# Kernel tuning notes

Hardware: AMD Instinct MI355X
Metric: run time of the kernel (lower is better)

The kernel has to match this reference:

```python
import jax, jax.numpy as jnp
import numpy as np

EPS = float(np.finfo(np.float32).eps)
LAMBDA = 0.01          # lambda_coeff
W_POS, W_NEG = 0.7, 0.3  # weights[0], weights[1]
BETA = 1.0             # function_dict['beta'] for 'exp'
N_GROUPS = 64          # number of categorical tuples
GROUP_W = 16           # width of each tuple (tup[1]-tup[0])
CAT_COLS = N_GROUPS * GROUP_W   # 1024 columns covered by tuples
HIDDEN, IN_FEATS = 1024, 2048   # model.layers[0].weight shape
BATCH = 8388608


def setup_inputs() -> dict:
    key = jax.random.key(0)
    k1, k2, k3 = jax.random.split(key, 3)
    p = jax.random.uniform(k1, (BATCH,), jnp.float32)
    y = (jax.random.uniform(k2, (BATCH,), jnp.float32) > 0.5).astype(jnp.float32)
    W = jax.random.normal(k3, (HIDDEN, IN_FEATS), jnp.float32) * 0.05
    return {"p": p, "y": y, "W": W}


def _f(x):
    # 'exp' penalty: 1 - exp(-x^2/beta) + |x|
    return 1.0 - jnp.exp(-(x * x) / BETA) + jnp.abs(x)


def reference(p, y, W):
    # weighted binary cross entropy with clamped probabilities
    log_p = jnp.log(jnp.clip(p, EPS, 1.0 - EPS))
    log_1mp = jnp.log(jnp.clip(1.0 - p, EPS, 1.0 - EPS))
    nll = -(W_POS * y * log_p + W_NEG * (1.0 - y) * log_1mp)
    bce = jnp.mean(nll)

    # per-column L2 norms of first-layer weight: [IN_FEATS]
    col_norm = jnp.sqrt(jnp.sum(W * W, axis=0))

    # tuple groups: mean of column norms within each group, then penalty f
    seg_ids = jnp.repeat(jnp.arange(N_GROUPS), GROUP_W)  # [CAT_COLS]
    group_mean = jax.ops.segment_sum(col_norm[:CAT_COLS], seg_ids,
                                     num_segments=N_GROUPS) / GROUP_W
    reg = jnp.sum(_f(group_mean)) + jnp.sum(_f(col_norm[CAT_COLS:]))

    return bce + reg * LAMBDA
```

## Files before the change

### kernel.cpp

```cpp
#include <hip/hip_runtime.h>
#include <math.h>

#define EPSC 1.1920928955078125e-07f
#define BATCH 8388608
#define IN_FEATS 2048
#define N_W_BLOCKS 128
#define N_BCE_BLOCKS 2048
#define N_SLOTS (N_W_BLOCKS + N_BCE_BLOCKS)
#define TOTAL_BLOCKS (1 + N_SLOTS)
#define BCE_ITERS 4
#define MAGIC 0x5EEDF00Du

__device__ __forceinline__ float penalty_f(float x) {
    return 1.0f - __expf(-x * x) + fabsf(x);
}

__device__ __forceinline__ float wave_reduce(float v) {
    #pragma unroll
    for (int o = 32; o > 0; o >>= 1) v += __shfl_down(v, o, 64);
    return v;
}

__device__ __forceinline__ void publish(unsigned long long* slot, float v) {
    unsigned long long w = ((unsigned long long)MAGIC << 32) | (unsigned long long)__float_as_uint(v);
    __hip_atomic_store(slot, w, __ATOMIC_RELAXED, __HIP_MEMORY_SCOPE_AGENT);
}

__global__ __launch_bounds__(256) void fused_k(
        const float* __restrict__ p, const float* __restrict__ y,
        const float* __restrict__ W,
        unsigned long long* __restrict__ slots,
        float* __restrict__ out) {
    const int b = blockIdx.x;
    const int t = threadIdx.x;

    if (b == 0) {
        float reg = 0.0f, bce = 0.0f;
        #pragma unroll
        for (int j = 0; j < (N_SLOTS + 255) / 256; ++j) {
            int i = t + j * 256;
            if (i < N_SLOTS) {
                unsigned long long w;
                do {
                    w = __hip_atomic_load(&slots[i], __ATOMIC_RELAXED,
                                          __HIP_MEMORY_SCOPE_AGENT);
                } while ((unsigned)(w >> 32) != MAGIC);
                float v = __uint_as_float((unsigned)(w & 0xFFFFFFFFu));
                if (i < N_W_BLOCKS) reg += v; else bce += v;
            }
        }
        reg = wave_reduce(reg);
        bce = wave_reduce(bce);
        __shared__ float wr[4], wb[4];
        if ((t & 63) == 0) { wr[t >> 6] = reg; wb[t >> 6] = bce; }
        __syncthreads();
        if (t == 0) {
            float R = (wr[0] + wr[1]) + (wr[2] + wr[3]);
            float B = (wb[0] + wb[1]) + (wb[2] + wb[3]);
            out[0] = B * (1.0f / (float)BATCH) + 0.01f * R;
        }
    } else if (b <= N_W_BLOCKS) {
        const int sb = b - 1;
        const int colbase = sb * 16;
        const int c4 = t & 3;
        const int rs = t >> 2;
        const float4* wbase = (const float4*)(W + (size_t)rs * IN_FEATS + colbase) + c4;
        float4 a = {0.f, 0.f, 0.f, 0.f};
        #pragma unroll
        for (int it = 0; it < 16; ++it) {
            float4 w = wbase[(size_t)it * 64 * (IN_FEATS / 4)];
            a.x = fmaf(w.x, w.x, a.x);
            a.y = fmaf(w.y, w.y, a.y);
            a.z = fmaf(w.z, w.z, a.z);
            a.w = fmaf(w.w, w.w, a.w);
        }
        __shared__ float lds[64][16];
        lds[rs][c4 * 4 + 0] = a.x;
        lds[rs][c4 * 4 + 1] = a.y;
        lds[rs][c4 * 4 + 2] = a.z;
        lds[rs][c4 * 4 + 3] = a.w;
        __syncthreads();

        __shared__ float ln[16];
        if (t < 16) {
            float s = 0.0f;
            #pragma unroll 8
            for (int r = 0; r < 64; ++r) s += lds[r][t];
            ln[t] = sqrtf(s);
        }
        __syncthreads();
        if (t == 0) {
            float contrib;
            if (sb < 64) {
                float gs = 0.0f;
                #pragma unroll
                for (int k = 0; k < 16; ++k) gs += ln[k];
                contrib = penalty_f(gs * (1.0f / 16.0f));
            } else {
                float s = 0.0f;
                #pragma unroll
                for (int k = 0; k < 16; ++k) s += penalty_f(ln[k]);
                contrib = s;
            }
            publish(&slots[sb], contrib);
        }
    } else {
        const int bb = b - 1 - N_W_BLOCKS;
        const float4* p4 = (const float4*)p + (size_t)bb * 1024;
        const float4* y4 = (const float4*)y + (size_t)bb * 1024;

        float4 pv[BCE_ITERS], yv[BCE_ITERS];
        #pragma unroll
        for (int it = 0; it < BCE_ITERS; ++it) {
            int i = it * 256 + t;
            pv[it] = p4[i];
            yv[it] = y4[i];
        }
        float acc = 0.0f;
        #pragma unroll
        for (int it = 0; it < BCE_ITERS; ++it) {
            float pp[4] = {pv[it].x, pv[it].y, pv[it].z, pv[it].w};
            float yy[4] = {yv[it].x, yv[it].y, yv[it].z, yv[it].w};
            #pragma unroll
            for (int k = 0; k < 4; ++k) {
                bool pos = yy[k] > 0.5f;
                float x  = pos ? pp[k] : 1.0f - pp[k];
                float w  = pos ? 0.7f : 0.3f;
                float xc = fminf(fmaxf(x, EPSC), 1.0f - EPSC);
                acc -= w * __logf(xc);
            }
        }
        acc = wave_reduce(acc);
        __shared__ float ws_[4];
        if ((t & 63) == 0) ws_[t >> 6] = acc;
        __syncthreads();
        if (t == 0) publish(&slots[N_W_BLOCKS + bb], ws_[0] + ws_[1] + ws_[2] + ws_[3]);
    }
}

extern "C" void kernel_launch(void* const* d_in, const int* in_sizes, int n_in,
                              void* d_out, int out_size, void* d_ws, size_t ws_size,
                              hipStream_t stream) {
    const float* p = (const float*)d_in[0];
    const float* y = (const float*)d_in[1];
    const float* W = (const float*)d_in[2];
    float* out = (float*)d_out;
    unsigned long long* slots = (unsigned long long*)d_ws;

    fused_k<<<TOTAL_BLOCKS, 256, 0, stream>>>(p, y, W, slots, out);
}
```

Before: 18.88 us.

## Split weight column-norm work into row-quarter blocks with cross-block partial handoff

The weight-norm stage is reorganised from 128 blocks each covering 16 columns over all rows into 256 blocks, each covering 32 columns over a quarter of the rows. Three of every four blocks publish per-column partial sums of squares to workspace slots, and the fourth polls for them and computes the norms and penalty. The goal is more memory-level parallelism per block, with loads issued up front so W is streamed by more blocks at once. Loads of W, p and y are also made nontemporal. The change adds inter-block spin-waits, which could stall if the finishing blocks are scheduled before their producers.

After: 15.37 us, median of 2. 1.23x faster.

```diff
diff --git a/kernel.cpp b/kernel.cpp
--- a/kernel.cpp
+++ b/kernel.cpp
@@ -1,13 +1,15 @@
 #include <hip/hip_runtime.h>
 #include <math.h>
+
+typedef float f32x4 __attribute__((ext_vector_type(4)));
 
 #define EPSC 1.1920928955078125e-07f
 #define BATCH 8388608
 #define IN_FEATS 2048
-#define N_W_BLOCKS 128
+#define N_STRIPS 64
+#define N_WQ_BLOCKS (N_STRIPS * 4)
 #define N_BCE_BLOCKS 2048
-#define N_SLOTS (N_W_BLOCKS + N_BCE_BLOCKS)
-#define TOTAL_BLOCKS (1 + N_SLOTS)
+#define TOTAL_BLOCKS (1 + N_WQ_BLOCKS + N_BCE_BLOCKS)
 #define BCE_ITERS 4
 #define MAGIC 0x5EEDF00Du
 
@@ -22,14 +24,25 @@
 }
 
 __device__ __forceinline__ void publish(unsigned long long* slot, float v) {
-    unsigned long long w = ((unsigned long long)MAGIC << 32) | (unsigned long long)__float_as_uint(v);
+    unsigned long long w = ((unsigned long long)MAGIC << 32)
+                         | (unsigned long long)__float_as_uint(v);
     __hip_atomic_store(slot, w, __ATOMIC_RELAXED, __HIP_MEMORY_SCOPE_AGENT);
+}
+
+__device__ __forceinline__ float poll(const unsigned long long* slot) {
+    unsigned long long w;
+    do {
+        w = __hip_atomic_load(slot, __ATOMIC_RELAXED, __HIP_MEMORY_SCOPE_AGENT);
+    } while ((unsigned)(w >> 32) != MAGIC);
+    return __uint_as_float((unsigned)(w & 0xFFFFFFFFu));
 }
 
 __global__ __launch_bounds__(256) void fused_k(
         const float* __restrict__ p, const float* __restrict__ y,
         const float* __restrict__ W,
-        unsigned long long* __restrict__ slots,
+        unsigned long long* __restrict__ bce_s,
+        unsigned long long* __restrict__ strip_s,
+        unsigned long long* __restrict__ csq_s,
         float* __restrict__ out) {
     const int b = blockIdx.x;
     const int t = threadIdx.x;
@@ -37,16 +50,11 @@
     if (b == 0) {
         float reg = 0.0f, bce = 0.0f;
         #pragma unroll
-        for (int j = 0; j < (N_SLOTS + 255) / 256; ++j) {
+        for (int j = 0; j < 9; ++j) {
             int i = t + j * 256;
-            if (i < N_SLOTS) {
-                unsigned long long w;
-                do {
-                    w = __hip_atomic_load(&slots[i], __ATOMIC_RELAXED,
-                                          __HIP_MEMORY_SCOPE_AGENT);
-                } while ((unsigned)(w >> 32) != MAGIC);
-                float v = __uint_as_float((unsigned)(w & 0xFFFFFFFFu));
-                if (i < N_W_BLOCKS) reg += v; else bce += v;
+            if (i < N_STRIPS + N_BCE_BLOCKS) {
+                if (i < N_STRIPS) reg += poll(&strip_s[i]);
+                else              bce += poll(&bce_s[i - N_STRIPS]);
             }
         }
         reg = wave_reduce(reg);
@@ -59,72 +67,81 @@
             float B = (wb[0] + wb[1]) + (wb[2] + wb[3]);
             out[0] = B * (1.0f / (float)BATCH) + 0.01f * R;
         }
-    } else if (b <= N_W_BLOCKS) {
-        const int sb = b - 1;
-        const int colbase = sb * 16;
-        const int c4 = t & 3;
-        const int rs = t >> 2;
-        const float4* wbase = (const float4*)(W + (size_t)rs * IN_FEATS + colbase) + c4;
-        float4 a = {0.f, 0.f, 0.f, 0.f};
-        #pragma unroll
-        for (int it = 0; it < 16; ++it) {
-            float4 w = wbase[(size_t)it * 64 * (IN_FEATS / 4)];
-            a.x = fmaf(w.x, w.x, a.x);
-            a.y = fmaf(w.y, w.y, a.y);
-            a.z = fmaf(w.z, w.z, a.z);
-            a.w = fmaf(w.w, w.w, a.w);
+    } else if (b <= N_WQ_BLOCKS) {
+        const int wqb = b - 1;
+        const int s = wqb >> 2;
+        const int q = wqb & 3;
+        const int f4 = t & 7;
+        const int r0 = t >> 3;
+        const f32x4* Wb = (const f32x4*)W
+                        + (size_t)(q * 256) * (IN_FEATS / 4) + s * 8 + f4;
+        f32x4 a = {0.f, 0.f, 0.f, 0.f};
+        {
+            f32x4 w[8];
+            #pragma unroll
+            for (int i = 0; i < 8; ++i)
+                w[i] = __builtin_nontemporal_load(Wb + (size_t)(r0 + 32 * i) * (IN_FEATS / 4));
+            #pragma unroll
+            for (int i = 0; i < 8; ++i) a = w[i] * w[i] + a;
         }
-        __shared__ float lds[64][16];
-        lds[rs][c4 * 4 + 0] = a.x;
-        lds[rs][c4 * 4 + 1] = a.y;
-        lds[rs][c4 * 4 + 2] = a.z;
-        lds[rs][c4 * 4 + 3] = a.w;
+        __shared__ f32x4 l4[32][8];
+        l4[r0][f4] = a;
         __syncthreads();
 
-        __shared__ float ln[16];
-        if (t < 16) {
-            float s = 0.0f;
+        __shared__ float lnb[32];
+        if (t < 32) {
+            const float* lf = (const float*)l4;
+            float cs = 0.0f;
             #pragma unroll 8
-            for (int r = 0; r < 64; ++r) s += lds[r][t];
-            ln[t] = sqrtf(s);
+            for (int r = 0; r < 32; ++r) cs += lf[r * 32 + t];
+            if (q < 3) {
+                publish(&csq_s[(s * 3 + q) * 32 + t], cs);
+            } else {
+                float total = cs;
+                #pragma unroll
+                for (int qq = 0; qq < 3; ++qq)
+                    total += poll(&csq_s[(s * 3 + qq) * 32 + t]);
+                lnb[t] = sqrtf(total);
+            }
         }
         __syncthreads();
-        if (t == 0) {
+        if (q == 3 && t == 0) {
             float contrib;
-            if (sb < 64) {
-                float gs = 0.0f;
+            if (s < 32) {
+                float g0 = 0.0f, g1 = 0.0f;
                 #pragma unroll
-                for (int k = 0; k < 16; ++k) gs += ln[k];
-                contrib = penalty_f(gs * (1.0f / 16.0f));
+                for (int k = 0; k < 16; ++k) { g0 += lnb[k]; g1 += lnb[16 + k]; }
+                contrib = penalty_f(g0 * (1.0f / 16.0f))
+                        + penalty_f(g1 * (1.0f / 16.0f));
             } else {
-                float s = 0.0f;
+                float sum = 0.0f;
                 #pragma unroll
-                for (int k = 0; k < 16; ++k) s += penalty_f(ln[k]);
-                contrib = s;
+                for (int k = 0; k < 32; ++k) sum += penalty_f(lnb[k]);
+                contrib = sum;
             }
-            publish(&slots[sb], contrib);
+            publish(&strip_s[s], contrib);
         }
     } else {
-        const int bb = b - 1 - N_W_BLOCKS;
-        const float4* p4 = (const float4*)p + (size_t)bb * 1024;
-        const float4* y4 = (const float4*)y + (size_t)bb * 1024;
+        const int bb = b - 1 - N_WQ_BLOCKS;
+        const f32x4* p4 = (const f32x4*)p + (size_t)bb * 1024;
+        const f32x4* y4 = (const f32x4*)y + (size_t)bb * 1024;
 
-        float4 pv[BCE_ITERS], yv[BCE_ITERS];
+        f32x4 pv[BCE_ITERS], yv[BCE_ITERS];
         #pragma unroll
         for (int it = 0; it < BCE_ITERS; ++it) {
             int i = it * 256 + t;
-            pv[it] = p4[i];
-            yv[it] = y4[i];
+            pv[it] = __builtin_nontemporal_load(p4 + i);
+            yv[it] = __builtin_nontemporal_load(y4 + i);
         }
         float acc = 0.0f;
         #pragma unroll
         for (int it = 0; it < BCE_ITERS; ++it) {
-            float pp[4] = {pv[it].x, pv[it].y, pv[it].z, pv[it].w};
-            float yy[4] = {yv[it].x, yv[it].y, yv[it].z, yv[it].w};
             #pragma unroll
             for (int k = 0; k < 4; ++k) {
-                bool pos = yy[k] > 0.5f;
-                float x  = pos ? pp[k] : 1.0f - pp[k];
+                float pk = pv[it][k];
+                float yk = yv[it][k];
+                bool pos = yk > 0.5f;
+                float x  = pos ? pk : 1.0f - pk;
                 float w  = pos ? 0.7f : 0.3f;
                 float xc = fminf(fmaxf(x, EPSC), 1.0f - EPSC);
                 acc -= w * __logf(xc);
@@ -134,7 +151,7 @@
         __shared__ float ws_[4];
         if ((t & 63) == 0) ws_[t >> 6] = acc;
         __syncthreads();
-        if (t == 0) publish(&slots[N_W_BLOCKS + bb], ws_[0] + ws_[1] + ws_[2] + ws_[3]);
+        if (t == 0) publish(&bce_s[bb], ws_[0] + ws_[1] + ws_[2] + ws_[3]);
     }
 }
 
@@ -145,7 +162,10 @@
     const float* y = (const float*)d_in[1];
     const float* W = (const float*)d_in[2];
     float* out = (float*)d_out;
-    unsigned long long* slots = (unsigned long long*)d_ws;
 
-    fused_k<<<TOTAL_BLOCKS, 256, 0, stream>>>(p, y, W, slots, out);
+    unsigned long long* bce_s   = (unsigned long long*)d_ws;
+    unsigned long long* strip_s = bce_s + N_BCE_BLOCKS;
+    unsigned long long* csq_s   = strip_s + N_STRIPS;
+
+    fused_k<<<TOTAL_BLOCKS, 256, 0, stream>>>(p, y, W, bce_s, strip_s, csq_s, out);
 }
```
